# Kernel tuning notes

Hardware: AMD Instinct MI355X
Metric: run time of the kernel (lower is better)

## Reference

```python
import jax, jax.numpy as jnp
import numpy as np
import math

D_MODEL = 1024
NHEAD = 16
HEAD_DIM = D_MODEL // NHEAD  # 64
R_HEAD = 8  # r // nhead = 128 // 16


def setup_inputs() -> dict:
    key = jax.random.key(0)
    ks = jax.random.split(key, 6)
    b, s = 2, 2048
    scale = 1.0 / math.sqrt(D_MODEL)
    return {
        "x": jax.random.normal(ks[0], (b, s, D_MODEL), dtype=jnp.float32),
        "Wq": jax.random.normal(ks[1], (D_MODEL, D_MODEL), dtype=jnp.float32) * scale,
        "Wk": jax.random.normal(ks[2], (D_MODEL, D_MODEL), dtype=jnp.float32) * scale,
        "Wv": jax.random.normal(ks[3], (D_MODEL, D_MODEL), dtype=jnp.float32) * scale,
        "Wo": jax.random.normal(ks[4], (D_MODEL, D_MODEL), dtype=jnp.float32) * scale,
        "B": jax.random.normal(ks[5], (D_MODEL, R_HEAD), dtype=jnp.float32),
    }


def reference(x, Wq, Wk, Wv, Wo, B):
    b, s, d = x.shape
    # Linear projections (torch nn.Linear: y = x @ W.T)
    Q = (x @ Wq.T).reshape(b, s, NHEAD, HEAD_DIM).transpose(0, 2, 1, 3)  # [b,h,s,hd]
    K = (x @ Wk.T).reshape(b, s, NHEAD, HEAD_DIM).transpose(0, 2, 1, 3)
    V = (x @ Wv.T).reshape(b, s, NHEAD, HEAD_DIM).transpose(0, 2, 1, 3)
    # Shared basis: head h uses rows [h*head_dim : (h+1)*head_dim] of B
    B_heads = B.reshape(NHEAD, HEAD_DIM, R_HEAD)  # [h,hd,r]
    # Low-rank projected queries/keys (vectorized form of the per-head loop)
    Qr = jnp.einsum('bhsd,hdr->bhsr', Q, B_heads)  # [b,h,s,r]
    Kr = jnp.einsum('bhsd,hdr->bhsr', K, B_heads)
    scores = jnp.einsum('bhqr,bhkr->bhqk', Qr, Kr) / math.sqrt(R_HEAD)  # [b,h,s,s]
    attn = jax.nn.softmax(scores, axis=-1)  # dropout is identity in eval
    out = jnp.einsum('bhqk,bhkd->bhqd', attn, V)  # [b,h,s,hd]
    out = out.transpose(0, 2, 1, 3).reshape(b, s, d)
    return out @ Wo.T
```

## Files before the change

### kernel.cpp

```cpp
#include <hip/hip_runtime.h>

#define SEQ 2048
#define DM 1024

typedef __attribute__((ext_vector_type(8))) short bs8;
typedef __attribute__((ext_vector_type(4))) float vf4;
typedef __attribute__((ext_vector_type(4))) unsigned int vu4;

__device__ __forceinline__ unsigned short bf16u(float f) {
  unsigned int u = __float_as_uint(f);
  u = (u + 0x7fffu + ((u >> 16) & 1u)) >> 16;
  return (unsigned short)u;
}

__device__ __forceinline__ unsigned int cvt_pk(float lo, float hi) {
  unsigned int r;
  asm("v_cvt_pk_bf16_f32 %0, %1, %2" : "=v"(r) : "v"(lo), "v"(hi));
  return r;
}

__device__ __forceinline__ float fexp2(float x) {
  float r;
  asm("v_exp_f32 %0, %1" : "=v"(r) : "v"(x));
  return r;
}

__device__ __forceinline__ void gload16(const unsigned short* g, unsigned short* l) {
  __builtin_amdgcn_global_load_lds(
      (const __attribute__((address_space(1))) unsigned int*)g,
      (__attribute__((address_space(3))) unsigned int*)l, 16, 0, 0);
}

__global__ void k_combine(const float* __restrict__ Wq, const float* __restrict__ Wk,
                          const float* __restrict__ Bm, float* __restrict__ Cqk) {
  int e = blockIdx.x * 256 + threadIdx.x;
  int which = e >> 17;
  int rem = e & 131071;
  int hr = rem >> 10;
  int j = rem & 1023;
  int h = hr >> 3, r = hr & 7;
  const float* W = which ? Wk : Wq;
  float acc = 0.f;
  #pragma unroll 8
  for (int d = 0; d < 64; d++) {
    int gd = h * 64 + d;
    acc += Bm[gd * 8 + r] * W[gd * 1024 + j];
  }
  Cqk[(size_t)(which * 128 + hr) * 1024 + j] = acc;
}

__global__ void k_cvt(const float* __restrict__ in, unsigned short* __restrict__ out, int n4) {
  int i = blockIdx.x * 256 + threadIdx.x;
  if (i >= n4) return;
  float4 v = ((const float4*)in)[i];
  ushort4 o;
  o.x = bf16u(v.x); o.y = bf16u(v.y); o.z = bf16u(v.z); o.w = bf16u(v.w);
  ((ushort4*)out)[i] = o;
}

__global__ __launch_bounds__(256) void k_gemm_f32(const float* __restrict__ A,
    const float* __restrict__ W, float* __restrict__ C0, float* __restrict__ C1,
    int M, int N, int K) {
  __shared__ float As[32][68];
  __shared__ float Ws[32][68];
  int t = threadIdx.x;
  int m0 = blockIdx.x * 64, n0 = blockIdx.y * 64;
  int kz = blockIdx.z;
  float* C = kz ? C1 : C0;
  int tm = t >> 4, tn = t & 15;
  float acc[4][4];
  #pragma unroll
  for (int a = 0; a < 4; a++)
    #pragma unroll
    for (int b = 0; b < 4; b++) acc[a][b] = 0.f;

  for (int k0 = kz * 512; k0 < kz * 512 + 512; k0 += 32) {
    __syncthreads();
    #pragma unroll
    for (int i = 0; i < 2; i++) {
      int idx = t + 256 * i;
      int row = idx >> 3, c4 = idx & 7;
      float4 av = *(const float4*)&A[(size_t)(m0 + row) * K + k0 + c4 * 4];
      As[c4*4+0][row] = av.x; As[c4*4+1][row] = av.y;
      As[c4*4+2][row] = av.z; As[c4*4+3][row] = av.w;
      float4 wv = *(const float4*)&W[(size_t)(n0 + row) * K + k0 + c4 * 4];
      Ws[c4*4+0][row] = wv.x; Ws[c4*4+1][row] = wv.y;
      Ws[c4*4+2][row] = wv.z; Ws[c4*4+3][row] = wv.w;
    }
    __syncthreads();
    #pragma unroll
    for (int k = 0; k < 32; k++) {
      float4 a = *(const float4*)&As[k][tm * 4];
      float4 w = *(const float4*)&Ws[k][tn * 4];
      float av[4] = {a.x, a.y, a.z, a.w};
      float wv[4] = {w.x, w.y, w.z, w.w};
      #pragma unroll
      for (int rm = 0; rm < 4; rm++)
        #pragma unroll
        for (int cn = 0; cn < 4; cn++)
          acc[rm][cn] += av[rm] * wv[cn];
    }
  }
  #pragma unroll
  for (int rm = 0; rm < 4; rm++) {
    float4 o = {acc[rm][0], acc[rm][1], acc[rm][2], acc[rm][3]};
    *(float4*)&C[(size_t)(m0 + tm * 4 + rm) * N + n0 + tn * 4] = o;
  }
}

__global__ void k_hilo(const float* __restrict__ QA, const float* __restrict__ QB,
                       unsigned short* __restrict__ Qhl, unsigned short* __restrict__ Khl) {
  int i = blockIdx.x * 256 + threadIdx.x;
  int side = i >> 16;
  int nh = i & 65535;
  int n = nh & 4095;
  int h = nh >> 12;
  size_t off = (size_t)n * 256 + side * 128 + h * 8;
  const float sc = side ? 1.0f : (1.4426950408889634f * 0.35355339059327373f);
  unsigned short* dst = (side ? Khl : Qhl) + ((size_t)h * 4096 + n) * 16;
  float4 a0 = *(const float4*)&QA[off];
  float4 a1 = *(const float4*)&QA[off + 4];
  float4 b0 = *(const float4*)&QB[off];
  float4 b1 = *(const float4*)&QB[off + 4];
  float f[8] = {a0.x+b0.x, a0.y+b0.y, a0.z+b0.z, a0.w+b0.w,
                a1.x+b1.x, a1.y+b1.y, a1.z+b1.z, a1.w+b1.w};
  unsigned short hs[8], ls[8];
  #pragma unroll
  for (int j = 0; j < 8; j++) {
    float fs = f[j] * sc;
    unsigned short h16 = bf16u(fs);
    float hf = __uint_as_float(((unsigned int)h16) << 16);
    hs[j] = h16;
    ls[j] = bf16u(fs - hf);
  }
  uint4 hv = {(unsigned int)hs[0] | ((unsigned int)hs[1] << 16),
              (unsigned int)hs[2] | ((unsigned int)hs[3] << 16),
              (unsigned int)hs[4] | ((unsigned int)hs[5] << 16),
              (unsigned int)hs[6] | ((unsigned int)hs[7] << 16)};
  uint4 lv = {(unsigned int)ls[0] | ((unsigned int)ls[1] << 16),
              (unsigned int)ls[2] | ((unsigned int)ls[3] << 16),
              (unsigned int)ls[4] | ((unsigned int)ls[5] << 16),
              (unsigned int)ls[6] | ((unsigned int)ls[7] << 16)};
  *(uint4*)dst = hv;
  *(uint4*)(dst + 8) = lv;
}

template<int OUT>
__global__ __launch_bounds__(256) void k_gemm128(const unsigned short* __restrict__ A,
    const unsigned short* __restrict__ W, void* __restrict__ Cout, int M, int N, int K) {
  __shared__ unsigned short Ah[128 * 64];
  __shared__ unsigned short Bh[64 * 64];
  int t = threadIdx.x, lane = t & 63, w = t >> 6;
  int gg = lane >> 4, r = lane & 15;
  int m0 = blockIdx.x * 128, n0 = blockIdx.y * 64;
  vf4 acc[2][4];
  #pragma unroll
  for (int i = 0; i < 2; i++)
    #pragma unroll
    for (int j = 0; j < 4; j++) acc[i][j] = (vf4){0.f, 0.f, 0.f, 0.f};

  int prow = lane >> 3, pslot = lane & 7;
  const unsigned short* asrc[4];
  unsigned short* aldst[4];
  #pragma unroll
  for (int p = 0; p < 4; p++) {
    int rr = w * 32 + p * 8 + prow;
    int c = pslot ^ ((rr ^ (rr >> 3)) & 7);
    asrc[p] = &A[(size_t)(m0 + rr) * K + c * 8];
    aldst[p] = &Ah[(w * 32 + p * 8) * 64];
  }
  const unsigned short* bsrc[2];
  unsigned short* bldst[2];
  #pragma unroll
  for (int p = 0; p < 2; p++) {
    int rn = w * 16 + p * 8 + prow;
    int c = pslot ^ ((rn ^ (rn >> 3)) & 7);
    bsrc[p] = &W[(size_t)(n0 + rn) * K + c * 8];
    bldst[p] = &Bh[(w * 16 + p * 8) * 64];
  }

  int aoff[2][2], boff[4][2];
  #pragma unroll
  for (int fm = 0; fm < 2; fm++) {
    int arow = w * 32 + fm * 16 + r;
    int key = (arow ^ (arow >> 3)) & 7;
    #pragma unroll
    for (int kk = 0; kk < 2; kk++)
      aoff[fm][kk] = arow * 64 + ((kk * 4 + gg) ^ key) * 8;
  }
  #pragma unroll
  for (int fn = 0; fn < 4; fn++) {
    int brow = fn * 16 + r;
    int key = (brow ^ (brow >> 3)) & 7;
    #pragma unroll
    for (int kk = 0; kk < 2; kk++)
      boff[fn][kk] = brow * 64 + ((kk * 4 + gg) ^ key) * 8;
  }

  for (int k0 = 0; k0 < K; k0 += 64) {
    __syncthreads();
    #pragma unroll
    for (int p = 0; p < 4; p++) gload16(asrc[p] + k0, aldst[p]);
    #pragma unroll
    for (int p = 0; p < 2; p++) gload16(bsrc[p] + k0, bldst[p]);
    __syncthreads();
    bs8 af[2][2], bf[4][2];
    #pragma unroll
    for (int fm = 0; fm < 2; fm++)
      #pragma unroll
      for (int kk = 0; kk < 2; kk++) af[fm][kk] = *(const bs8*)&Ah[aoff[fm][kk]];
    #pragma unroll
    for (int fn = 0; fn < 4; fn++)
      #pragma unroll
      for (int kk = 0; kk < 2; kk++) bf[fn][kk] = *(const bs8*)&Bh[boff[fn][kk]];
    #pragma unroll
    for (int kk = 0; kk < 2; kk++)
      #pragma unroll
      for (int fm = 0; fm < 2; fm++)
        #pragma unroll
        for (int fn = 0; fn < 4; fn++)
          acc[fm][fn] = __builtin_amdgcn_mfma_f32_16x16x32_bf16(af[fm][kk], bf[fn][kk], acc[fm][fn], 0, 0, 0);
  }

  #pragma unroll
  for (int fm = 0; fm < 2; fm++)
    #pragma unroll
    for (int fn = 0; fn < 4; fn++) {
      if (OUT == 2) {
        int n = n0 + fn * 16 + r;
        int m = m0 + w * 32 + fm * 16 + gg * 4;
        ushort4 st = {bf16u(acc[fm][fn][0]), bf16u(acc[fm][fn][1]),
                      bf16u(acc[fm][fn][2]), bf16u(acc[fm][fn][3])};
        *(ushort4*)&((unsigned short*)Cout)[(size_t)n * M + m] = st;
      } else {
        #pragma unroll
        for (int j = 0; j < 4; j++) {
          int m = m0 + w * 32 + fm * 16 + gg * 4 + j;
          int n = n0 + fn * 16 + r;
          ((float*)Cout)[(size_t)m * N + n] = acc[fm][fn][j];
        }
      }
    }
}

__global__ __launch_bounds__(256, 4) void k_attn(const unsigned short* __restrict__ Qhl,
    const unsigned short* __restrict__ Khl, const unsigned short* __restrict__ Vt,
    unsigned short* __restrict__ AO) {
  int bx = blockIdx.x;
  int qt = bx & 31, h = (bx >> 5) & 15, b = bx >> 9;
  int t = threadIdx.x, lane = t & 63, w = t >> 6;
  int gg = lane >> 4, r = lane & 15;

  __shared__ unsigned short VT[2][4096];

  int qglob = b * 2048 + qt * 64 + w * 16 + r;
  bs8 bq = {0, 0, 0, 0, 0, 0, 0, 0};
  if (gg != 3)
    bq = *(const bs8*)&Qhl[((size_t)h * 4096 + qglob) * 16 + (gg == 2 ? 8 : 0)];

  const unsigned short* Khead = &Khl[((size_t)h * 4096 + (size_t)b * 2048) * 16];
  int koff = (gg == 1) ? 8 : 0;
  const unsigned short* kp[4];
  #pragma unroll
  for (int kt = 0; kt < 4; kt++) {
    int ks = (kt & 1) * 32 + (r >> 2) * 8 + (kt >> 1) * 4 + (r & 3);
    kp[kt] = Khead + (size_t)ks * 16 + koff;
  }

  int vrow = t >> 2, vcl = t & 3;
  const unsigned short* vsrc = &Vt[(size_t)(h * 64 + vrow) * 4096 + (size_t)b * 2048 + vcl * 16];
  int vkey = (vrow ^ (vrow >> 2)) & 7;
  int sw0 = ((vcl * 2) ^ vkey) * 8;
  int sw1 = ((vcl * 2 + 1) ^ vkey) * 8;

  int pvoff[2][4];
  #pragma unroll
  for (int sl = 0; sl < 2; sl++)
    #pragma unroll
    for (int fn = 0; fn < 4; fn++) {
      int row = 4 * r + fn;
      int key = (row ^ (row >> 2)) & 7;
      pvoff[sl][fn] = row * 64 + ((sl * 4 + gg) ^ key) * 8;
    }

  float mrun = -INFINITY;
  vf4 acc[4];
  #pragma unroll
  for (int i = 0; i < 4; i++) acc[i] = (vf4){0.f, 0.f, 0.f, 0.f};
  vf4 accs = (vf4){0.f, 0.f, 0.f, 0.f};

  const bs8 ones = (bs8){16256, 16256, 16256, 16256, 16256, 16256, 16256, 16256};

  uint4 fv0 = *(const uint4*)(vsrc);
  uint4 fv1 = *(const uint4*)(vsrc + 8);
  bs8 af0 = *(const bs8*)(kp[0]);
  bs8 af1 = *(const bs8*)(kp[1]);
  bs8 af2 = *(const bs8*)(kp[2]);
  bs8 af3 = *(const bs8*)(kp[3]);
  {
    unsigned short* vd = &VT[0][vrow * 64];
    *(uint4*)(vd + sw0) = fv0;
    *(uint4*)(vd + sw1) = fv1;
  }
  __syncthreads();

  #pragma unroll 2
  for (int kc = 0; kc < 32; kc++) {
    int nc = kc < 31 ? kc + 1 : 31;
    uint4 nv0 = *(const uint4*)(vsrc + nc * 64);
    uint4 nv1 = *(const uint4*)(vsrc + nc * 64 + 8);
    size_t nb16 = (size_t)nc * 64 * 16;
    bs8 naf0 = *(const bs8*)(kp[0] + nb16);
    bs8 naf1 = *(const bs8*)(kp[1] + nb16);
    bs8 naf2 = *(const bs8*)(kp[2] + nb16);
    bs8 naf3 = *(const bs8*)(kp[3] + nb16);

    vf4 z = (vf4){0.f, 0.f, 0.f, 0.f};
    __builtin_amdgcn_s_setprio(1);
    vf4 s0 = __builtin_amdgcn_mfma_f32_16x16x32_bf16(af0, bq, z, 0, 0, 0);
    vf4 s1 = __builtin_amdgcn_mfma_f32_16x16x32_bf16(af1, bq, z, 0, 0, 0);
    vf4 s2 = __builtin_amdgcn_mfma_f32_16x16x32_bf16(af2, bq, z, 0, 0, 0);
    vf4 s3 = __builtin_amdgcn_mfma_f32_16x16x32_bf16(af3, bq, z, 0, 0, 0);
    __builtin_amdgcn_s_setprio(0);

    float p[16];
    #pragma unroll
    for (int j = 0; j < 4; j++) {
      p[0 + j] = s0[j]; p[4 + j] = s1[j]; p[8 + j] = s2[j]; p[12 + j] = s3[j];
    }
    float cm0 = fmaxf(fmaxf(p[0],  p[1]),  p[2]);
    float cm1 = fmaxf(fmaxf(p[3],  p[4]),  p[5]);
    float cm2 = fmaxf(fmaxf(p[6],  p[7]),  p[8]);
    float cm3 = fmaxf(fmaxf(p[9],  p[10]), p[11]);
    float cm4 = fmaxf(fmaxf(p[12], p[13]), p[14]);
    float cmax = fmaxf(fmaxf(fmaxf(cm0, cm1), cm2),
                       fmaxf(fmaxf(cm3, cm4), p[15]));
    cmax = fmaxf(cmax, __shfl_xor(cmax, 16));
    cmax = fmaxf(cmax, __shfl_xor(cmax, 32));

    if (!__all(cmax <= mrun + 8.f)) {
      float mnew = fmaxf(mrun, cmax);
      float alpha = fexp2(mrun - mnew);
      float al[4];
      #pragma unroll
      for (int j = 0; j < 4; j++) al[j] = __shfl(alpha, gg * 4 + j);
      #pragma unroll
      for (int fn = 0; fn < 4; fn++) {
        acc[fn][0] *= al[0]; acc[fn][1] *= al[1];
        acc[fn][2] *= al[2]; acc[fn][3] *= al[3];
      }
      accs[0] *= al[0]; accs[1] *= al[1];
      accs[2] *= al[2]; accs[3] *= al[3];
      mrun = mnew;
    }

    #pragma unroll
    for (int i = 0; i < 16; i++) p[i] = fexp2(p[i] - mrun);

    vu4 a0 = {cvt_pk(p[0],  p[1]),  cvt_pk(p[2],  p[3]),
              cvt_pk(p[8],  p[9]),  cvt_pk(p[10], p[11])};
    vu4 a1 = {cvt_pk(p[4],  p[5]),  cvt_pk(p[6],  p[7]),
              cvt_pk(p[12], p[13]), cvt_pk(p[14], p[15])};
    bs8 apv0 = __builtin_bit_cast(bs8, a0);
    bs8 apv1 = __builtin_bit_cast(bs8, a1);

    const unsigned short* vb = &VT[kc & 1][0];
    __builtin_amdgcn_s_setprio(1);
    #pragma unroll
    for (int sl = 0; sl < 2; sl++) {
      bs8 a = sl ? apv1 : apv0;
      #pragma unroll
      for (int fn = 0; fn < 4; fn++) {
        bs8 bv = *(const bs8*)&vb[pvoff[sl][fn]];
        acc[fn] = __builtin_amdgcn_mfma_f32_16x16x32_bf16(a, bv, acc[fn], 0, 0, 0);
      }
    }
    accs = __builtin_amdgcn_mfma_f32_16x16x32_bf16(apv0, ones, accs, 0, 0, 0);
    accs = __builtin_amdgcn_mfma_f32_16x16x32_bf16(apv1, ones, accs, 0, 0, 0);
    __builtin_amdgcn_s_setprio(0);

    af0 = naf0; af1 = naf1; af2 = naf2; af3 = naf3;

    if (kc < 31) {
      unsigned short* vd = &VT[(kc + 1) & 1][vrow * 64];
      *(uint4*)(vd + sw0) = nv0;
      *(uint4*)(vd + sw1) = nv1;
      __syncthreads();
    }
  }

  float li[4];
  #pragma unroll
  for (int j = 0; j < 4; j++) li[j] = 1.f / accs[j];
  #pragma unroll
  for (int j = 0; j < 4; j++) {
    uint2 o;
    o.x = cvt_pk(acc[0][j] * li[j], acc[1][j] * li[j]);
    o.y = cvt_pk(acc[2][j] * li[j], acc[3][j] * li[j]);
    int qq = qt * 64 + w * 16 + gg * 4 + j;
    *(uint2*)&AO[((size_t)b * SEQ + qq) * 1024 + h * 64 + 4 * r] = o;
  }
}

extern "C" void kernel_launch(void* const* d_in, const int* in_sizes, int n_in,
                              void* d_out, int out_size, void* d_ws, size_t ws_size,
                              hipStream_t stream) {
  const float* x  = (const float*)d_in[0];
  const float* Wq = (const float*)d_in[1];
  const float* Wk = (const float*)d_in[2];
  const float* Wv = (const float*)d_in[3];
  const float* Wo = (const float*)d_in[4];
  const float* Bm = (const float*)d_in[5];
  float* out = (float*)d_out;

  char* ws = (char*)d_ws;
  float* Cqk  = (float*)ws;                    ws += (size_t)256 * 1024 * 4;
  float* QKrA = (float*)ws;                    ws += (size_t)4096 * 256 * 4;
  float* QKrB = (float*)ws;                    ws += (size_t)4096 * 256 * 4;
  unsigned short* xh  = (unsigned short*)ws;   ws += (size_t)4096 * 1024 * 2;
  unsigned short* Wvh = (unsigned short*)ws;   ws += (size_t)1024 * 1024 * 2;
  unsigned short* Woh = (unsigned short*)ws;   ws += (size_t)1024 * 1024 * 2;
  unsigned short* Vt  = (unsigned short*)ws;   ws += (size_t)4096 * 1024 * 2;
  unsigned short* AO  = (unsigned short*)ws;   ws += (size_t)4096 * 1024 * 2;
  unsigned short* Qhl = (unsigned short*)ws;   ws += (size_t)16 * 4096 * 16 * 2;
  unsigned short* Khl = (unsigned short*)ws;   ws += (size_t)16 * 4096 * 16 * 2;

  k_combine<<<1024, 256, 0, stream>>>(Wq, Wk, Bm, Cqk);
  k_cvt<<<4096, 256, 0, stream>>>(x,  xh,  1048576);
  k_cvt<<<1024, 256, 0, stream>>>(Wv, Wvh, 262144);
  k_cvt<<<1024, 256, 0, stream>>>(Wo, Woh, 262144);
  k_gemm_f32<<<dim3(64, 4, 2), 256, 0, stream>>>(x, Cqk, QKrA, QKrB, 4096, 256, 1024);
  k_hilo<<<512, 256, 0, stream>>>(QKrA, QKrB, Qhl, Khl);
  k_gemm128<2><<<dim3(32, 16), 256, 0, stream>>>(xh, Wvh, (void*)Vt, 4096, 1024, 1024);
  k_attn<<<1024, 256, 0, stream>>>(Qhl, Khl, Vt, AO);
  k_gemm128<0><<<dim3(32, 16), 256, 0, stream>>>(AO, Woh, (void*)out, 4096, 1024, 1024);
}
```

Measured before the change: 139.7 us.

## Replace fp32 SIMT low-rank QK projection GEMM with split-bf16 MFMA GEMM

```diff
diff --git a/kernel.cpp b/kernel.cpp
--- a/kernel.cpp
+++ b/kernel.cpp
@@ -32,7 +32,8 @@
 }
 
 __global__ void k_combine(const float* __restrict__ Wq, const float* __restrict__ Wk,
-                          const float* __restrict__ Bm, float* __restrict__ Cqk) {
+                          const float* __restrict__ Bm,
+                          unsigned short* __restrict__ Ch, unsigned short* __restrict__ Cl) {
   int e = blockIdx.x * 256 + threadIdx.x;
   int which = e >> 17;
   int rem = e & 131071;
@@ -46,7 +47,11 @@
     int gd = h * 64 + d;
     acc += Bm[gd * 8 + r] * W[gd * 1024 + j];
   }
-  Cqk[(size_t)(which * 128 + hr) * 1024 + j] = acc;
+  size_t idx = (size_t)(which * 128 + hr) * 1024 + j;
+  unsigned short h16 = bf16u(acc);
+  float hf = __uint_as_float(((unsigned int)h16) << 16);
+  Ch[idx] = h16;
+  Cl[idx] = bf16u(acc - hf);
 }
 
 __global__ void k_cvt(const float* __restrict__ in, unsigned short* __restrict__ out, int n4) {
@@ -58,54 +63,117 @@
   ((ushort4*)out)[i] = o;
 }
 
-__global__ __launch_bounds__(256) void k_gemm_f32(const float* __restrict__ A,
-    const float* __restrict__ W, float* __restrict__ C0, float* __restrict__ C1,
-    int M, int N, int K) {
-  __shared__ float As[32][68];
-  __shared__ float Ws[32][68];
-  int t = threadIdx.x;
+__global__ void k_cvt_hl(const float* __restrict__ in, unsigned short* __restrict__ oh,
+                         unsigned short* __restrict__ ol, int n4) {
+  int i = blockIdx.x * 256 + threadIdx.x;
+  if (i >= n4) return;
+  float4 v = ((const float4*)in)[i];
+  float f[4] = {v.x, v.y, v.z, v.w};
+  ushort4 hv, lv;
+  unsigned short hs[4], ls[4];
+  #pragma unroll
+  for (int j = 0; j < 4; j++) {
+    unsigned short h16 = bf16u(f[j]);
+    float hf = __uint_as_float(((unsigned int)h16) << 16);
+    hs[j] = h16;
+    ls[j] = bf16u(f[j] - hf);
+  }
+  hv.x = hs[0]; hv.y = hs[1]; hv.z = hs[2]; hv.w = hs[3];
+  lv.x = ls[0]; lv.y = ls[1]; lv.z = ls[2]; lv.w = ls[3];
+  ((ushort4*)oh)[i] = hv;
+  ((ushort4*)ol)[i] = lv;
+}
+
+__global__ __launch_bounds__(256) void k_qkr(
+    const unsigned short* __restrict__ Xh, const unsigned short* __restrict__ Xl,
+    const unsigned short* __restrict__ Bh_, const unsigned short* __restrict__ Bl_,
+    float* __restrict__ C0, float* __restrict__ C1) {
+  const int K = 1024, N = 256;
+  __shared__ unsigned short Sah[64 * 64];
+  __shared__ unsigned short Sal[64 * 64];
+  __shared__ unsigned short Sbh[64 * 64];
+  __shared__ unsigned short Sbl[64 * 64];
+  int t = threadIdx.x, lane = t & 63, w = t >> 6;
+  int gg = lane >> 4, r = lane & 15;
   int m0 = blockIdx.x * 64, n0 = blockIdx.y * 64;
   int kz = blockIdx.z;
   float* C = kz ? C1 : C0;
-  int tm = t >> 4, tn = t & 15;
-  float acc[4][4];
-  #pragma unroll
-  for (int a = 0; a < 4; a++)
-    #pragma unroll
-    for (int b = 0; b < 4; b++) acc[a][b] = 0.f;
-
-  for (int k0 = kz * 512; k0 < kz * 512 + 512; k0 += 32) {
+  vf4 acc[4];
+  #pragma unroll
+  for (int fn = 0; fn < 4; fn++) acc[fn] = (vf4){0.f, 0.f, 0.f, 0.f};
+
+  int prow = lane >> 3, pslot = lane & 7;
+  const unsigned short *ah_src[2], *al_src[2], *bh_src[2], *bl_src[2];
+  unsigned short *ah_dst[2], *al_dst[2], *bh_dst[2], *bl_dst[2];
+  #pragma unroll
+  for (int p = 0; p < 2; p++) {
+    int rr = w * 16 + p * 8 + prow;
+    int c = pslot ^ ((rr ^ (rr >> 3)) & 7);
+    size_t ga = (size_t)(m0 + rr) * K + (size_t)kz * 512 + c * 8;
+    ah_src[p] = Xh + ga;  al_src[p] = Xl + ga;
+    size_t gb = (size_t)(n0 + rr) * K + (size_t)kz * 512 + c * 8;
+    bh_src[p] = Bh_ + gb; bl_src[p] = Bl_ + gb;
+    int ldo = (w * 16 + p * 8) * 64;
+    ah_dst[p] = &Sah[ldo]; al_dst[p] = &Sal[ldo];
+    bh_dst[p] = &Sbh[ldo]; bl_dst[p] = &Sbl[ldo];
+  }
+
+  int aoff[2], boff[4][2];
+  {
+    int arow = w * 16 + r;
+    int key = (arow ^ (arow >> 3)) & 7;
+    #pragma unroll
+    for (int kk = 0; kk < 2; kk++) aoff[kk] = arow * 64 + ((kk * 4 + gg) ^ key) * 8;
+  }
+  #pragma unroll
+  for (int fn = 0; fn < 4; fn++) {
+    int brow = fn * 16 + r;
+    int key = (brow ^ (brow >> 3)) & 7;
+    #pragma unroll
+    for (int kk = 0; kk < 2; kk++) boff[fn][kk] = brow * 64 + ((kk * 4 + gg) ^ key) * 8;
+  }
+
+  for (int k0 = 0; k0 < 512; k0 += 64) {
     __syncthreads();
     #pragma unroll
-    for (int i = 0; i < 2; i++) {
-      int idx = t + 256 * i;
-      int row = idx >> 3, c4 = idx & 7;
-      float4 av = *(const float4*)&A[(size_t)(m0 + row) * K + k0 + c4 * 4];
-      As[c4*4+0][row] = av.x; As[c4*4+1][row] = av.y;
-      As[c4*4+2][row] = av.z; As[c4*4+3][row] = av.w;
-      float4 wv = *(const float4*)&W[(size_t)(n0 + row) * K + k0 + c4 * 4];
-      Ws[c4*4+0][row] = wv.x; Ws[c4*4+1][row] = wv.y;
-      Ws[c4*4+2][row] = wv.z; Ws[c4*4+3][row] = wv.w;
+    for (int p = 0; p < 2; p++) {
+      gload16(ah_src[p] + k0, ah_dst[p]);
+      gload16(al_src[p] + k0, al_dst[p]);
+      gload16(bh_src[p] + k0, bh_dst[p]);
+      gload16(bl_src[p] + k0, bl_dst[p]);
     }
     __syncthreads();
-    #pragma unroll
-    for (int k = 0; k < 32; k++) {
-      float4 a = *(const float4*)&As[k][tm * 4];
-      float4 w = *(const float4*)&Ws[k][tn * 4];
-      float av[4] = {a.x, a.y, a.z, a.w};
-      float wv[4] = {w.x, w.y, w.z, w.w};
-      #pragma unroll
-      for (int rm = 0; rm < 4; rm++)
-        #pragma unroll
-        for (int cn = 0; cn < 4; cn++)
-          acc[rm][cn] += av[rm] * wv[cn];
-    }
-  }
-  #pragma unroll
-  for (int rm = 0; rm < 4; rm++) {
-    float4 o = {acc[rm][0], acc[rm][1], acc[rm][2], acc[rm][3]};
-    *(float4*)&C[(size_t)(m0 + tm * 4 + rm) * N + n0 + tn * 4] = o;
-  }
+    bs8 afh[2], afl[2], bfh[4][2], bfl[4][2];
+    #pragma unroll
+    for (int kk = 0; kk < 2; kk++) {
+      afh[kk] = *(const bs8*)&Sah[aoff[kk]];
+      afl[kk] = *(const bs8*)&Sal[aoff[kk]];
+    }
+    #pragma unroll
+    for (int fn = 0; fn < 4; fn++)
+      #pragma unroll
+      for (int kk = 0; kk < 2; kk++) {
+        bfh[fn][kk] = *(const bs8*)&Sbh[boff[fn][kk]];
+        bfl[fn][kk] = *(const bs8*)&Sbl[boff[fn][kk]];
+      }
+    #pragma unroll
+    for (int kk = 0; kk < 2; kk++)
+      #pragma unroll
+      for (int fn = 0; fn < 4; fn++) {
+        acc[fn] = __builtin_amdgcn_mfma_f32_16x16x32_bf16(afh[kk], bfh[fn][kk], acc[fn], 0, 0, 0);
+        acc[fn] = __builtin_amdgcn_mfma_f32_16x16x32_bf16(afh[kk], bfl[fn][kk], acc[fn], 0, 0, 0);
+        acc[fn] = __builtin_amdgcn_mfma_f32_16x16x32_bf16(afl[kk], bfh[fn][kk], acc[fn], 0, 0, 0);
+      }
+  }
+
+  #pragma unroll
+  for (int fn = 0; fn < 4; fn++)
+    #pragma unroll
+    for (int j = 0; j < 4; j++) {
+      int m = m0 + w * 16 + gg * 4 + j;
+      int n = n0 + fn * 16 + r;
+      C[(size_t)m * N + n] = acc[fn][j];
+    }
 }
 
 __global__ void k_hilo(const float* __restrict__ QA, const float* __restrict__ QB,
@@ -414,7 +482,8 @@
   float* out = (float*)d_out;
 
   char* ws = (char*)d_ws;
-  float* Cqk  = (float*)ws;                    ws += (size_t)256 * 1024 * 4;
+  unsigned short* Cqkh = (unsigned short*)ws;  ws += (size_t)256 * 1024 * 2;
+  unsigned short* Cqkl = (unsigned short*)ws;  ws += (size_t)256 * 1024 * 2;
   float* QKrA = (float*)ws;                    ws += (size_t)4096 * 256 * 4;
   float* QKrB = (float*)ws;                    ws += (size_t)4096 * 256 * 4;
   unsigned short* xh  = (unsigned short*)ws;   ws += (size_t)4096 * 1024 * 2;
@@ -424,12 +493,13 @@
   unsigned short* AO  = (unsigned short*)ws;   ws += (size_t)4096 * 1024 * 2;
   unsigned short* Qhl = (unsigned short*)ws;   ws += (size_t)16 * 4096 * 16 * 2;
   unsigned short* Khl = (unsigned short*)ws;   ws += (size_t)16 * 4096 * 16 * 2;
-
-  k_combine<<<1024, 256, 0, stream>>>(Wq, Wk, Bm, Cqk);
-  k_cvt<<<4096, 256, 0, stream>>>(x,  xh,  1048576);
+  unsigned short* xl = AO;
+
+  k_combine<<<1024, 256, 0, stream>>>(Wq, Wk, Bm, Cqkh, Cqkl);
+  k_cvt_hl<<<4096, 256, 0, stream>>>(x, xh, xl, 1048576);
   k_cvt<<<1024, 256, 0, stream>>>(Wv, Wvh, 262144);
   k_cvt<<<1024, 256, 0, stream>>>(Wo, Woh, 262144);
-  k_gemm_f32<<<dim3(64, 4, 2), 256, 0, stream>>>(x, Cqk, QKrA, QKrB, 4096, 256, 1024);
+  k_qkr<<<dim3(64, 4, 2), 256, 0, stream>>>(xh, xl, Cqkh, Cqkl, QKrA, QKrB);
   k_hilo<<<512, 256, 0, stream>>>(QKrA, QKrB, Qhl, Khl);
   k_gemm128<2><<<dim3(32, 16), 256, 0, stream>>>(xh, Wvh, (void*)Vt, 4096, 1024, 1024);
   k_attn<<<1024, 256, 0, stream>>>(Qhl, Khl, Vt, AO);
```

New measurement: 118.1 us. -15.4%, faster.
